# Performance work log

Hardware: AMD Instinct MI355X
Metric: run time of the kernel (lower is better)

## Reference

```python
import jax, jax.numpy as jnp
import numpy as np

S, B, V = 128, 64, 32000
EH, EO, H, O = 512, 512, 1024, 1024
THRESH = 1e-06


def _thresh(x):
    # nn.Threshold(1e-6, 0): x if x > 1e-6 else 0
    return jnp.where(x > THRESH, x, 0.0)


def setup_inputs() -> dict:
    key = jax.random.key(0)
    ks = jax.random.split(key, 12)
    ids = jax.random.randint(ks[0], (S, B), 0, V, dtype=jnp.int32)
    s = 0.02
    return {
        "ids": ids,
        "W1": jax.random.normal(ks[1], (EH, V), jnp.float32) * s,
        "b1": jax.random.normal(ks[2], (EH,), jnp.float32) * s,
        "W2": jax.random.normal(ks[3], (EO, EH), jnp.float32) * s,
        "b2": jax.random.normal(ks[4], (EO,), jnp.float32) * s,
        "W_ih": jax.random.normal(ks[5], (3 * H, EO), jnp.float32) * s,
        "b_ih": jax.random.normal(ks[6], (3 * H,), jnp.float32) * s,
        "W_hh": jax.random.normal(ks[7], (3 * H, H), jnp.float32) * s,
        "b_hh": jax.random.normal(ks[8], (3 * H,), jnp.float32) * s,
        "W_out": jax.random.normal(ks[9], (O, H), jnp.float32) * s,
        "b_out": jax.random.normal(ks[10], (O,), jnp.float32) * s,
    }


def reference(ids, W1, b1, W2, b2, W_ih, b_ih, W_hh, b_hh, W_out, b_out):
    # one_hot(ids, V) @ W1.T + b1 == exact gather of W1 columns (sum of zeros is exact)
    emb = _thresh(jnp.take(W1.T, ids, axis=0) + b1)            # [S, B, EH]
    x = _thresh(jnp.einsum('sbe,oe->sbo', emb, W2) + b2)       # [S, B, EO]
    # Precompute all input-gate projections in one GEMM
    xW = jnp.einsum('sbe,ge->sbg', x, W_ih) + b_ih             # [S, B, 3H]

    def step(h, xw):
        gh = h @ W_hh.T + b_hh                                 # [B, 3H]
        xr, xz, xn = jnp.split(xw, 3, axis=-1)
        hr, hz, hn = jnp.split(gh, 3, axis=-1)
        r = jax.nn.sigmoid(xr + hr)
        z = jax.nn.sigmoid(xz + hz)
        n = jnp.tanh(xn + r * hn)
        h_new = (1.0 - z) * n + z * h
        return h_new, None

    h0 = jnp.zeros((B, H), dtype=x.dtype)
    hT, _ = jax.lax.scan(step, h0, xW)                         # [B, H]
    # Dropout is identity in inference; final Linear
    out = hT @ W_out.T + b_out                                 # [B, O]
    return out[None]                                           # [1, B, O] (h_n layout)
```

## Files before the change

kernel.cpp:

```cpp
#include <hip/hip_runtime.h>
#include <stdint.h>
#include <stddef.h>

#define S_LEN 128
#define B_SZ  64
#define V_SZ  32000
#define EH    512
#define EO    512
#define H_SZ  1024
#define O_SZ  1024
#define G3    3072

typedef __attribute__((ext_vector_type(8))) short short8;
typedef __attribute__((ext_vector_type(4))) float floatx4;
typedef __attribute__((ext_vector_type(8))) unsigned short ushortx8;
typedef __attribute__((ext_vector_type(4))) unsigned uintx4;

__device__ __forceinline__ unsigned short f2bf(float f) {
  unsigned u = __builtin_bit_cast(unsigned, f);
  u += 0x7FFFu + ((u >> 16) & 1u);
  return (unsigned short)(u >> 16);
}
__device__ __forceinline__ float bf2f(unsigned short h) {
  unsigned u = ((unsigned)h) << 16;
  return __builtin_bit_cast(float, u);
}

__device__ __forceinline__ void gld_lds16(const void* g, void* l) {
  __builtin_amdgcn_global_load_lds((const __attribute__((address_space(1))) void*)g,
                                   (__attribute__((address_space(3))) void*)l, 16, 0, 0);
}

__global__ __launch_bounds__(256) void cvt3_bf16(const float* __restrict__ a,
                                                 const float* __restrict__ b,
                                                 const float* __restrict__ c,
                                                 unsigned short* __restrict__ out) {
  const int na4 = (EO * EH) / 4;
  const int nb4 = (G3 * EO) / 4;
  int i = blockIdx.x * 256 + threadIdx.x;
  const float* src;
  int off;
  if (i < na4)            { src = a; off = i; }
  else if (i < na4 + nb4) { src = b; off = i - na4; }
  else                    { src = c; off = i - na4 - nb4; }
  float4 v = ((const float4*)src)[off];
  ushort4 o;
  o.x = f2bf(v.x); o.y = f2bf(v.y); o.z = f2bf(v.z); o.w = f2bf(v.w);
  ((ushort4*)out)[i] = o;
}

__global__ __launch_bounds__(256) void transpose_w1_bf16(const float* __restrict__ W1,
                                                         unsigned short* __restrict__ W1T) {
  __shared__ unsigned short tile[64][72];
  int t = threadIdx.x;
  int v0 = blockIdx.x * 64;
  int e0 = blockIdx.y * 64;
  for (int i = 0; i < 4; ++i) {
    int e = (t >> 4) + i * 16;
    int v = (t & 15) * 4;
    float4 w = *(const float4*)&W1[(size_t)(e0 + e) * V_SZ + v0 + v];
    tile[v + 0][e] = f2bf(w.x);
    tile[v + 1][e] = f2bf(w.y);
    tile[v + 2][e] = f2bf(w.z);
    tile[v + 3][e] = f2bf(w.w);
  }
  __syncthreads();
  for (int i = 0; i < 2; ++i) {
    int v = (t >> 3) + i * 32;
    int e = (t & 7) * 8;
    ushortx8 o;
    for (int j = 0; j < 8; ++j) o[j] = tile[v][e + j];
    *(ushortx8*)&W1T[(size_t)(v0 + v) * EH + e0 + e] = o;
  }
}

__global__ __launch_bounds__(256) void gather_emb(const int* __restrict__ ids,
                                                  const unsigned short* __restrict__ W1T,
                                                  const float* __restrict__ b1,
                                                  unsigned short* __restrict__ emb) {
  int t = threadIdx.x;
  int tok = blockIdx.x * 4 + (t >> 6);
  int lane = t & 63;
  int id = ids[tok];
  ushortx8 w = *(const ushortx8*)&W1T[(size_t)id * EH + lane * 8];
  float4 blo = *(const float4*)&b1[lane * 8];
  float4 bhi = *(const float4*)&b1[lane * 8 + 4];
  float bv[8] = {blo.x, blo.y, blo.z, blo.w, bhi.x, bhi.y, bhi.z, bhi.w};
  ushortx8 o;
  for (int j = 0; j < 8; ++j) {
    float x = bf2f(w[j]) + bv[j];
    x = (x > 1e-6f) ? x : 0.0f;
    o[j] = f2bf(x);
  }
  *(ushortx8*)&emb[(size_t)tok * EH + lane * 8] = o;
}

template <int ACT, int OUT_BF16>
__global__ __launch_bounds__(256) void gemm_bt(const unsigned short* __restrict__ A,
                                               const unsigned short* __restrict__ B,
                                               const float* __restrict__ bias,
                                               void* __restrict__ Cout,
                                               int M, int N, int K) {
  __shared__ unsigned short lA[128 * 64];
  __shared__ unsigned short lB[128 * 64];
  int t = threadIdx.x;
  int lane = t & 63;
  int wave = t >> 6;
  int bn = blockIdx.x, bm = blockIdx.y;
  int wm = (wave >> 1) * 64;
  int wn = (wave & 1) * 64;
  floatx4 acc[4][4] = {};

  int srow = t >> 3;
  int sslot = (t & 7) ^ (srow & 7);
  int scol = sslot * 8;

  const unsigned short* aptr[4];
  const unsigned short* bptr[4];
#pragma unroll
  for (int p = 0; p < 4; ++p) {
    int gra = bm * 128 + p * 32 + srow;  if (gra >= M) gra = M - 1;
    aptr[p] = A + (size_t)gra * K + scol;
    bptr[p] = B + (size_t)(bn * 128 + p * 32 + srow) * K + scol;
  }

  for (int k0 = 0; k0 < K; k0 += 64) {
    __syncthreads();
#pragma unroll
    for (int p = 0; p < 4; ++p) {
      gld_lds16(aptr[p] + k0, &lA[p * 2048 + t * 8]);
      gld_lds16(bptr[p] + k0, &lB[p * 2048 + t * 8]);
    }
    __syncthreads();
#pragma unroll
    for (int kk = 0; kk < 2; ++kk) {
      short8 af[4], bfr[4];
#pragma unroll
      for (int i = 0; i < 4; ++i) {
        int row = wm + i * 16 + (lane & 15);
        int phys = (kk * 4 + (lane >> 4)) ^ (row & 7);
        af[i] = *(const short8*)&lA[row * 64 + phys * 8];
      }
#pragma unroll
      for (int j = 0; j < 4; ++j) {
        int row = wn + j * 16 + (lane & 15);
        int phys = (kk * 4 + (lane >> 4)) ^ (row & 7);
        bfr[j] = *(const short8*)&lB[row * 64 + phys * 8];
      }
#pragma unroll
      for (int i = 0; i < 4; ++i)
#pragma unroll
        for (int j = 0; j < 4; ++j)
          acc[i][j] = __builtin_amdgcn_mfma_f32_16x16x32_bf16(af[i], bfr[j], acc[i][j], 0, 0, 0);
    }
  }

  int rowq = (lane >> 4) * 4;
  for (int j = 0; j < 4; ++j) {
    int col = bn * 128 + wn + j * 16 + (lane & 15);
    float bv = bias[col];
    for (int i = 0; i < 4; ++i) {
      int row0 = bm * 128 + wm + i * 16 + rowq;
      for (int r = 0; r < 4; ++r) {
        int row = row0 + r;
        if (row < M) {
          float v = acc[i][j][r] + bv;
          if (ACT) v = (v > 1e-6f) ? v : 0.0f;
          if (OUT_BF16) ((unsigned short*)Cout)[(size_t)row * N + col] = f2bf(v);
          else          ((float*)Cout)[(size_t)row * N + col] = v;
        }
      }
    }
  }
}

__global__ __launch_bounds__(256) void prep_whh(const float* __restrict__ W_hh,
                                                unsigned short* __restrict__ Wprep) {
  int tid = blockIdx.x * 256 + threadIdx.x;
  int lane = tid & 63;
  int c = tid >> 6;
  int cg = c / 96;
  int r  = c % 96;
  int g  = r >> 5;
  int t  = r & 31;
  int row = g * H_SZ + cg * 16 + (lane & 15);
  int k   = t * 32 + (lane >> 4) * 8;
  const float* src = &W_hh[(size_t)row * H_SZ + k];
  float4 v0 = *(const float4*)src;
  float4 v1 = *(const float4*)(src + 4);
  ushortx8 o;
  o[0] = f2bf(v0.x); o[1] = f2bf(v0.y); o[2] = f2bf(v0.z); o[3] = f2bf(v0.w);
  o[4] = f2bf(v1.x); o[5] = f2bf(v1.y); o[6] = f2bf(v1.z); o[7] = f2bf(v1.w);
  ((ushortx8*)Wprep)[tid] = o;
}

__global__ __launch_bounds__(256) void gru_persist(const unsigned short* __restrict__ hprep0,
                                                   unsigned short* __restrict__ hprep1,
                                                   unsigned short* __restrict__ hbfinal,
                                                   const unsigned short* __restrict__ Wprep,
                                                   const float* __restrict__ b_hh,
                                                   const unsigned short* __restrict__ xW,
                                                   unsigned* __restrict__ bar) {
  __shared__ unsigned short lB[96 * 512];
  __shared__ float lgh[3][4][256];
  __shared__ float lhf[256];
  int t = threadIdx.x;
  int lane = t & 63;
  int w = t >> 6;
  int bg = blockIdx.x >> 6;
  int cg = blockIdx.x & 63;

  const unsigned short* wsrc = Wprep + (size_t)cg * 96 * 512;
  for (int i = 0; i < 24; ++i) {
    int c = w * 24 + i;
    gld_lds16(wsrc + (size_t)c * 512 + lane * 8, &lB[c * 512 + lane * 8]);
  }
  lhf[t] = 0.0f;

  int b_loc = t >> 4;
  int j_loc = t & 15;
  int jcol = cg * 16 + j_loc;
  int bglob = bg * 16 + b_loc;
  float bhr = b_hh[jcol];
  float bhz = b_hh[H_SZ + jcol];
  float bhn = b_hh[2 * H_SZ + jcol];
  int tt2 = jcol >> 5;
  int q   = (jcol >> 3) & 3;
  int jj  = jcol & 7;
  int Ls  = b_loc | (q << 4);
  size_t hw_off32 = ((((size_t)(bg * 32 + tt2) * 64 + Ls) * 8) + (jj & ~1)) >> 1;

  const unsigned short* hbufs[2] = {hprep0, hprep1};
  unsigned* barp = bar + bg * 64;
  __syncthreads();

  for (int s = 0; s < S_LEN; ++s) {
    const unsigned short* hr = hbufs[s & 1];
    unsigned* hw32 = (unsigned*)hbufs[(s + 1) & 1];

    uintx4 av[8];
#pragma unroll
    for (int i = 0; i < 8; ++i) {
      int tt = w * 8 + i;
      const void* ap = hr + ((size_t)(bg * 32 + tt) * 64 + lane) * 8;
      asm volatile("global_load_dwordx4 %0, %1, off sc1" : "=v"(av[i]) : "v"(ap));
    }
    const unsigned short* xs = xW + (size_t)s * B_SZ * G3 + (size_t)bglob * G3;
    float xr = bf2f(xs[jcol]);
    float xz = bf2f(xs[H_SZ + jcol]);
    float xn = bf2f(xs[2 * H_SZ + jcol]);
    asm volatile("s_waitcnt vmcnt(0)"
                 : "+v"(av[0]), "+v"(av[1]), "+v"(av[2]), "+v"(av[3]),
                   "+v"(av[4]), "+v"(av[5]), "+v"(av[6]), "+v"(av[7])
                 :: "memory");

    floatx4 acc[3] = {};
#pragma unroll
    for (int i = 0; i < 8; ++i) {
      int tt = w * 8 + i;
      short8 a = __builtin_bit_cast(short8, av[i]);
#pragma unroll
      for (int g = 0; g < 3; ++g) {
        short8 bfr = *(const short8*)&lB[((g * 32 + tt) * 64 + lane) * 8];
        acc[g] = __builtin_amdgcn_mfma_f32_16x16x32_bf16(a, bfr, acc[g], 0, 0, 0);
      }
    }
#pragma unroll
    for (int g = 0; g < 3; ++g)
#pragma unroll
      for (int r = 0; r < 4; ++r)
        lgh[g][w][((lane >> 4) * 4 + r) * 16 + (lane & 15)] = acc[g][r];
    __syncthreads();

    float ghr = lgh[0][0][t] + lgh[0][1][t] + lgh[0][2][t] + lgh[0][3][t] + bhr;
    float ghz = lgh[1][0][t] + lgh[1][1][t] + lgh[1][2][t] + lgh[1][3][t] + bhz;
    float ghn = lgh[2][0][t] + lgh[2][1][t] + lgh[2][2][t] + lgh[2][3][t] + bhn;
    float rr = 1.0f / (1.0f + __expf(-(xr + ghr)));
    float zz = 1.0f / (1.0f + __expf(-(xz + ghz)));
    float nn = tanhf(xn + rr * ghn);
    float ho = lhf[t];
    float hnew = (1.0f - zz) * nn + zz * ho;
    lhf[t] = hnew;

    unsigned hb = (unsigned)f2bf(hnew);
    unsigned other = (unsigned)__shfl_xor((int)hb, 1);
    if ((jj & 1) == 0) {
      unsigned packed = hb | (other << 16);
      __hip_atomic_store(hw32 + hw_off32, packed,
                         __ATOMIC_RELAXED, __HIP_MEMORY_SCOPE_AGENT);
    }
    if (s == S_LEN - 1) hbfinal[(size_t)bglob * H_SZ + jcol] = (unsigned short)hb;

    if (s < S_LEN - 1) {
      __syncthreads();
      if (t == 0) {
        __hip_atomic_fetch_add(barp, 1u, __ATOMIC_RELAXED, __HIP_MEMORY_SCOPE_AGENT);
        unsigned target = 64u * (unsigned)(s + 1);
        while (__hip_atomic_load(barp, __ATOMIC_RELAXED, __HIP_MEMORY_SCOPE_AGENT) < target)
          __builtin_amdgcn_s_sleep(2);
      }
      __syncthreads();
    }
  }
}

extern "C" void kernel_launch(void* const* d_in, const int* in_sizes, int n_in,
                              void* d_out, int out_size, void* d_ws, size_t ws_size,
                              hipStream_t stream) {
  const int*   ids   = (const int*)d_in[0];
  const float* W1    = (const float*)d_in[1];
  const float* b1    = (const float*)d_in[2];
  const float* W2    = (const float*)d_in[3];
  const float* b2    = (const float*)d_in[4];
  const float* W_ih  = (const float*)d_in[5];
  const float* b_ih  = (const float*)d_in[6];
  const float* W_hh  = (const float*)d_in[7];
  const float* b_hh  = (const float*)d_in[8];
  const float* W_out = (const float*)d_in[9];
  const float* b_out = (const float*)d_in[10];
  float* out = (float*)d_out;

  uint8_t* wsp = (uint8_t*)d_ws;
  auto alloc = [&](size_t bytes) {
    uint8_t* p = wsp;
    wsp += (bytes + 255) & ~(size_t)255;
    return p;
  };
  unsigned short* W1T   = (unsigned short*)alloc((size_t)V_SZ * EH * 2);
  unsigned short* W2b   = (unsigned short*)alloc((size_t)EO * EH * 2);
  unsigned short* Wihb  = (unsigned short*)alloc((size_t)G3 * EO * 2);
  unsigned short* Woutb = (unsigned short*)alloc((size_t)O_SZ * H_SZ * 2);
  unsigned short* Wprep = (unsigned short*)alloc((size_t)G3 * H_SZ * 2);
  unsigned short* emb   = (unsigned short*)alloc((size_t)S_LEN * B_SZ * EH * 2);
  unsigned short* x     = (unsigned short*)alloc((size_t)S_LEN * B_SZ * EO * 2);
  unsigned short* xW    = (unsigned short*)alloc((size_t)S_LEN * B_SZ * G3 * 2);
  unsigned short* hprep0 = (unsigned short*)alloc((size_t)B_SZ * H_SZ * 2);
  unsigned short* hprep1 = (unsigned short*)alloc((size_t)B_SZ * H_SZ * 2);
  unsigned short* hbfinal = (unsigned short*)alloc((size_t)B_SZ * H_SZ * 2);
  unsigned*       bar     = (unsigned*)alloc(1024);

  cvt3_bf16<<<dim3(2816), 256, 0, stream>>>(W2, W_ih, W_out, W2b);

  prep_whh<<<dim3(1536), 256, 0, stream>>>(W_hh, Wprep);

  hipMemsetAsync(hprep0, 0, (size_t)B_SZ * H_SZ * 2, stream);
  hipMemsetAsync(bar, 0, 1024, stream);

  transpose_w1_bf16<<<dim3(V_SZ / 64, EH / 64), 256, 0, stream>>>(W1, W1T);

  gather_emb<<<dim3(S_LEN * B_SZ / 4), 256, 0, stream>>>(ids, W1T, b1, emb);

  gemm_bt<1, 1><<<dim3(EO / 128, S_LEN * B_SZ / 128), 256, 0, stream>>>(
      emb, W2b, b2, x, S_LEN * B_SZ, EO, EH);

  gemm_bt<0, 1><<<dim3(G3 / 128, S_LEN * B_SZ / 128), 256, 0, stream>>>(
      x, Wihb, b_ih, xW, S_LEN * B_SZ, G3, EO);

  {
    void* args[] = {(void*)&hprep0, (void*)&hprep1, (void*)&hbfinal,
                    (void*)&Wprep, (void*)&b_hh, (void*)&xW, (void*)&bar};
    hipLaunchCooperativeKernel((const void*)gru_persist, dim3(256), dim3(256),
                               args, 0, stream);
  }

  gemm_bt<0, 0><<<dim3(O_SZ / 128, 1), 256, 0, stream>>>(
      hbfinal, Woutb, b_out, out, B_SZ, O_SZ, H_SZ);
}
```

Before: 652.5 us.

## Fuse input-gate projection into persistent GRU kernel, overlapping with barrier wait

Removes the separate xW GEMM and its large intermediate buffer. Each persistent GRU block now keeps a pre-swizzled bf16 slice of W_ih in LDS, and three of its four waves compute the next step's input-gate projection with MFMA while wave 0 spins on the inter-block barrier. The hidden state master copy moves from LDS into a register. The intent is to hide the x-projection inside barrier latency and cut HBM traffic, at the cost of more LDS use and per-step global reads of x on the sequential critical path.

```diff
diff --git a/kernel.cpp b/kernel.cpp
--- a/kernel.cpp
+++ b/kernel.cpp
@@ -31,18 +31,15 @@
                                    (__attribute__((address_space(3))) void*)l, 16, 0, 0);
 }
 
-__global__ __launch_bounds__(256) void cvt3_bf16(const float* __restrict__ a,
+__global__ __launch_bounds__(256) void cvt2_bf16(const float* __restrict__ a,
                                                  const float* __restrict__ b,
-                                                 const float* __restrict__ c,
                                                  unsigned short* __restrict__ out) {
   const int na4 = (EO * EH) / 4;
-  const int nb4 = (G3 * EO) / 4;
   int i = blockIdx.x * 256 + threadIdx.x;
   const float* src;
   int off;
-  if (i < na4)            { src = a; off = i; }
-  else if (i < na4 + nb4) { src = b; off = i - na4; }
-  else                    { src = c; off = i - na4 - nb4; }
+  if (i < na4) { src = a; off = i; }
+  else         { src = b; off = i - na4; }
   float4 v = ((const float4*)src)[off];
   ushort4 o;
   o.x = f2bf(v.x); o.y = f2bf(v.y); o.z = f2bf(v.z); o.w = f2bf(v.w);
@@ -194,16 +191,39 @@
   ((ushortx8*)Wprep)[tid] = o;
 }
 
+__global__ __launch_bounds__(256) void prep_wih(const float* __restrict__ W_ih,
+                                                unsigned short* __restrict__ Wihp) {
+  int tid = blockIdx.x * 256 + threadIdx.x;
+  int lane = tid & 63;
+  int c = tid >> 6;
+  int cg = c / 48;
+  int r  = c % 48;
+  int g  = r >> 4;
+  int kq = r & 15;
+  int row = g * H_SZ + cg * 16 + (lane & 15);
+  int k   = kq * 32 + (lane >> 4) * 8;
+  const float* src = &W_ih[(size_t)row * EO + k];
+  float4 v0 = *(const float4*)src;
+  float4 v1 = *(const float4*)(src + 4);
+  ushortx8 o;
+  o[0] = f2bf(v0.x); o[1] = f2bf(v0.y); o[2] = f2bf(v0.z); o[3] = f2bf(v0.w);
+  o[4] = f2bf(v1.x); o[5] = f2bf(v1.y); o[6] = f2bf(v1.z); o[7] = f2bf(v1.w);
+  ((ushortx8*)Wihp)[tid] = o;
+}
+
 __global__ __launch_bounds__(256) void gru_persist(const unsigned short* __restrict__ hprep0,
                                                    unsigned short* __restrict__ hprep1,
                                                    unsigned short* __restrict__ hbfinal,
                                                    const unsigned short* __restrict__ Wprep,
+                                                   const unsigned short* __restrict__ Wihp,
                                                    const float* __restrict__ b_hh,
-                                                   const unsigned short* __restrict__ xW,
+                                                   const float* __restrict__ b_ih,
+                                                   const unsigned short* __restrict__ x,
                                                    unsigned* __restrict__ bar) {
   __shared__ unsigned short lB[96 * 512];
+  __shared__ unsigned short lWih[48 * 512];
   __shared__ float lgh[3][4][256];
-  __shared__ float lhf[256];
+  __shared__ float lgx[3][256];
   int t = threadIdx.x;
   int lane = t & 63;
   int w = t >> 6;
@@ -215,7 +235,11 @@
     int c = w * 24 + i;
     gld_lds16(wsrc + (size_t)c * 512 + lane * 8, &lB[c * 512 + lane * 8]);
   }
-  lhf[t] = 0.0f;
+  const unsigned short* wxs = Wihp + (size_t)cg * 48 * 512;
+  for (int i = 0; i < 12; ++i) {
+    int c = w * 12 + i;
+    gld_lds16(wxs + (size_t)c * 512 + lane * 8, &lWih[c * 512 + lane * 8]);
+  }
 
   int b_loc = t >> 4;
   int j_loc = t & 15;
@@ -224,6 +248,9 @@
   float bhr = b_hh[jcol];
   float bhz = b_hh[H_SZ + jcol];
   float bhn = b_hh[2 * H_SZ + jcol];
+  float bihr = b_ih[jcol];
+  float bihz = b_ih[H_SZ + jcol];
+  float bihn = b_ih[2 * H_SZ + jcol];
   int tt2 = jcol >> 5;
   int q   = (jcol >> 3) & 3;
   int jj  = jcol & 7;
@@ -232,7 +259,32 @@
 
   const unsigned short* hbufs[2] = {hprep0, hprep1};
   unsigned* barp = bar + bg * 64;
+  float hmaster = 0.0f;
+
+  auto xw_compute = [&](int sn) {
+    int g = w - 1;
+    const unsigned short* xrow =
+        x + ((size_t)(sn * B_SZ + bg * 16 + (lane & 15))) * EO + (lane >> 4) * 8;
+    floatx4 accx = {};
+#pragma unroll
+    for (int kq = 0; kq < 16; ++kq) {
+      uintx4 xv = *(const uintx4*)(xrow + kq * 32);
+      short8 a = __builtin_bit_cast(short8, xv);
+      short8 bfr = *(const short8*)&lWih[((g * 16 + kq) * 64 + lane) * 8];
+      accx = __builtin_amdgcn_mfma_f32_16x16x32_bf16(a, bfr, accx, 0, 0, 0);
+    }
+#pragma unroll
+    for (int r = 0; r < 4; ++r)
+      lgx[g][((lane >> 4) * 4 + r) * 16 + (lane & 15)] = accx[r];
+  };
+
   __syncthreads();
+
+  if (w >= 1) xw_compute(0);
+  __syncthreads();
+  float xr = lgx[0][t] + bihr;
+  float xz = lgx[1][t] + bihz;
+  float xn = lgx[2][t] + bihn;
 
   for (int s = 0; s < S_LEN; ++s) {
     const unsigned short* hr = hbufs[s & 1];
@@ -245,10 +297,6 @@
       const void* ap = hr + ((size_t)(bg * 32 + tt) * 64 + lane) * 8;
       asm volatile("global_load_dwordx4 %0, %1, off sc1" : "=v"(av[i]) : "v"(ap));
     }
-    const unsigned short* xs = xW + (size_t)s * B_SZ * G3 + (size_t)bglob * G3;
-    float xr = bf2f(xs[jcol]);
-    float xz = bf2f(xs[H_SZ + jcol]);
-    float xn = bf2f(xs[2 * H_SZ + jcol]);
     asm volatile("s_waitcnt vmcnt(0)"
                  : "+v"(av[0]), "+v"(av[1]), "+v"(av[2]), "+v"(av[3]),
                    "+v"(av[4]), "+v"(av[5]), "+v"(av[6]), "+v"(av[7])
@@ -278,9 +326,8 @@
     float rr = 1.0f / (1.0f + __expf(-(xr + ghr)));
     float zz = 1.0f / (1.0f + __expf(-(xz + ghz)));
     float nn = tanhf(xn + rr * ghn);
-    float ho = lhf[t];
-    float hnew = (1.0f - zz) * nn + zz * ho;
-    lhf[t] = hnew;
+    float hnew = (1.0f - zz) * nn + zz * hmaster;
+    hmaster = hnew;
 
     unsigned hb = (unsigned)f2bf(hnew);
     unsigned other = (unsigned)__shfl_xor((int)hb, 1);
@@ -293,13 +340,20 @@
 
     if (s < S_LEN - 1) {
       __syncthreads();
-      if (t == 0) {
-        __hip_atomic_fetch_add(barp, 1u, __ATOMIC_RELAXED, __HIP_MEMORY_SCOPE_AGENT);
-        unsigned target = 64u * (unsigned)(s + 1);
-        while (__hip_atomic_load(barp, __ATOMIC_RELAXED, __HIP_MEMORY_SCOPE_AGENT) < target)
-          __builtin_amdgcn_s_sleep(2);
+      if (w == 0) {
+        if (t == 0) {
+          __hip_atomic_fetch_add(barp, 1u, __ATOMIC_RELAXED, __HIP_MEMORY_SCOPE_AGENT);
+          unsigned target = 64u * (unsigned)(s + 1);
+          while (__hip_atomic_load(barp, __ATOMIC_RELAXED, __HIP_MEMORY_SCOPE_AGENT) < target)
+            __builtin_amdgcn_s_sleep(2);
+        }
+      } else {
+        xw_compute(s + 1);
       }
       __syncthreads();
+      xr = lgx[0][t] + bihr;
+      xz = lgx[1][t] + bihz;
+      xn = lgx[2][t] + bihn;
     }
   }
 }
@@ -328,20 +382,20 @@
   };
   unsigned short* W1T   = (unsigned short*)alloc((size_t)V_SZ * EH * 2);
   unsigned short* W2b   = (unsigned short*)alloc((size_t)EO * EH * 2);
-  unsigned short* Wihb  = (unsigned short*)alloc((size_t)G3 * EO * 2);
   unsigned short* Woutb = (unsigned short*)alloc((size_t)O_SZ * H_SZ * 2);
   unsigned short* Wprep = (unsigned short*)alloc((size_t)G3 * H_SZ * 2);
+  unsigned short* Wihp  = (unsigned short*)alloc((size_t)G3 * EO * 2);
   unsigned short* emb   = (unsigned short*)alloc((size_t)S_LEN * B_SZ * EH * 2);
   unsigned short* x     = (unsigned short*)alloc((size_t)S_LEN * B_SZ * EO * 2);
-  unsigned short* xW    = (unsigned short*)alloc((size_t)S_LEN * B_SZ * G3 * 2);
   unsigned short* hprep0 = (unsigned short*)alloc((size_t)B_SZ * H_SZ * 2);
   unsigned short* hprep1 = (unsigned short*)alloc((size_t)B_SZ * H_SZ * 2);
   unsigned short* hbfinal = (unsigned short*)alloc((size_t)B_SZ * H_SZ * 2);
   unsigned*       bar     = (unsigned*)alloc(1024);
 
-  cvt3_bf16<<<dim3(2816), 256, 0, stream>>>(W2, W_ih, W_out, W2b);
+  cvt2_bf16<<<dim3(1280), 256, 0, stream>>>(W2, W_out, W2b);
 
   prep_whh<<<dim3(1536), 256, 0, stream>>>(W_hh, Wprep);
+  prep_wih<<<dim3(768), 256, 0, stream>>>(W_ih, Wihp);
 
   hipMemsetAsync(hprep0, 0, (size_t)B_SZ * H_SZ * 2, stream);
   hipMemsetAsync(bar, 0, 1024, stream);
@@ -353,12 +407,10 @@
   gemm_bt<1, 1><<<dim3(EO / 128, S_LEN * B_SZ / 128), 256, 0, stream>>>(
       emb, W2b, b2, x, S_LEN * B_SZ, EO, EH);
 
-  gemm_bt<0, 1><<<dim3(G3 / 128, S_LEN * B_SZ / 128), 256, 0, stream>>>(
-      x, Wihb, b_ih, xW, S_LEN * B_SZ, G3, EO);
-
   {
     void* args[] = {(void*)&hprep0, (void*)&hprep1, (void*)&hbfinal,
-                    (void*)&Wprep, (void*)&b_hh, (void*)&xW, (void*)&bar};
+                    (void*)&Wprep, (void*)&Wihp, (void*)&b_hh, (void*)&b_ih,
+                    (void*)&x, (void*)&bar};
     hipLaunchCooperativeKernel((const void*)gru_persist, dim3(256), dim3(256),
                                args, 0, stream);
   }
```

Result: slower. 699.0 us (+7.1%).
